# Kernel optimization log

Hardware: AMD Instinct MI355X
Metric: run time of the kernel (lower is better)

Reference implementation:

```python
import jax, jax.numpy as jnp
import numpy as np

B, T, C, H = 4, 2048, 768, 12
D = C // H  # head dim = 64


def setup_inputs() -> dict:
    key = jax.random.key(0)
    ks = jax.random.split(key, 4)
    scale = 0.02
    return {
        "x": jax.random.normal(ks[0], (B, T, C), dtype=jnp.float32),
        "W_attn": jax.random.normal(ks[1], (C, 3 * C), dtype=jnp.float32) * scale,
        "b_attn": jnp.zeros((3 * C,), dtype=jnp.float32),
        "W_proj": jax.random.normal(ks[2], (C, C), dtype=jnp.float32) * scale,
        "b_proj": jnp.zeros((C,), dtype=jnp.float32),
    }


def reference(x, W_attn, b_attn, W_proj, b_proj):
    Bsz, Tlen, Cdim = x.shape
    qkv = x @ W_attn + b_attn                    # [B,T,3C]
    q, k, v = jnp.split(qkv, 3, axis=-1)          # each [B,T,C]
    # [B,T,C] -> [B,H,T,D]
    def heads(t):
        return t.reshape(Bsz, Tlen, H, D).transpose(0, 2, 1, 3)
    q, k, v = heads(q), heads(k), heads(v)
    att = jnp.einsum("bhqd,bhkd->bhqk", q, k) * (1.0 / np.sqrt(D))
    # causal mask: position q attends to k <= q
    mask = jnp.tril(jnp.ones((Tlen, Tlen), dtype=bool))
    att = jnp.where(mask[None, None], att, -jnp.inf)
    att = jax.nn.softmax(att, axis=-1)
    y = jnp.einsum("bhqk,bhkd->bhqd", att, v)     # [B,H,T,D]
    y = y.transpose(0, 2, 1, 3).reshape(Bsz, Tlen, Cdim)
    return y @ W_proj + b_proj
```

## Files before the change

kernel.cpp:

```cpp
#include <hip/hip_runtime.h>

#define B_SZ   4
#define T_LEN  2048
#define C_DIM  768
#define H_NUM  12
#define THREEC (3 * C_DIM)

typedef _Float16 f16;
typedef _Float16 half8 __attribute__((ext_vector_type(8)));
typedef _Float16 half4 __attribute__((ext_vector_type(4)));
typedef __fp16   pk2   __attribute__((ext_vector_type(2)));
typedef float    f32x4 __attribute__((ext_vector_type(4)));

#define GLD16(gaddr, laddr)                                                         \
  __builtin_amdgcn_global_load_lds(                                                 \
      (const __attribute__((address_space(1))) unsigned int*)(gaddr),               \
      (__attribute__((address_space(3))) unsigned int*)(laddr), 16, 0, 0)
#define MFMA16(a, b, c) __builtin_amdgcn_mfma_f32_16x16x32_f16(a, b, c, 0, 0, 0)

__global__ __launch_bounds__(256) void cast_f32_f16_kernel(
    const float* __restrict__ src, f16* __restrict__ dst, int n8) {
  int i = blockIdx.x * 256 + threadIdx.x;
  if (i >= n8) return;
  const float* s = src + (size_t)i * 8;
  half8 h;
#pragma unroll
  for (int u = 0; u < 8; ++u) h[u] = (f16)s[u];
  *(half8*)(dst + (size_t)i * 8) = h;
}

__global__ __launch_bounds__(256) void transpose_cast2_kernel(
    const float* __restrict__ Wa, const float* __restrict__ Wp,
    f16* __restrict__ WtA, f16* __restrict__ WtP) {
  __shared__ f16 tile[32][33];
  int bx = blockIdx.x;
  const float* W; f16* Wt; int N;
  if (bx < THREEC / 32) { W = Wa; Wt = WtA; N = THREEC; }
  else { W = Wp; Wt = WtP; N = C_DIM; bx -= THREEC / 32; }
  const int n0 = bx * 32, k0 = blockIdx.y * 32;
  const int tx = threadIdx.x & 31, ty = threadIdx.x >> 5;
#pragma unroll
  for (int i = 0; i < 4; ++i)
    tile[ty + i * 8][tx] = (f16)W[(size_t)(k0 + ty + i * 8) * N + n0 + tx];
  __syncthreads();
#pragma unroll
  for (int i = 0; i < 4; ++i)
    Wt[(size_t)(n0 + ty + i * 8) * C_DIM + k0 + tx] = tile[tx][ty + i * 8];
}

template <int BM, int BN, int OUT_F16>
__global__ __launch_bounds__(256) void gemm_f16_kernel(
    const f16* __restrict__ A, const f16* __restrict__ Bt,
    const float* __restrict__ bias, f16* __restrict__ OutH,
    float* __restrict__ OutF, int M, int N, int K) {
  __shared__ f16 As[BM * 64];
  __shared__ f16 Bs[BN * 64];
  const int tid = threadIdx.x;
  const int lane = tid & 63, wave = tid >> 6;
  const int lm = lane & 15, kq = lane >> 4, lm7 = lm & 7;
  constexpr int MT = BM / 32, NT = BN / 32;
  const int wm = (wave & 1) * (BM / 2), wn = (wave >> 1) * (BN / 2);
  const int row0 = blockIdx.y * BM, col0 = blockIdx.x * BN;

  f32x4 acc[MT][NT] = {};

  for (int k0 = 0; k0 < K; k0 += 64) {
    __syncthreads();
#pragma unroll
    for (int i = 0; i < BM / 32; ++i) {
      int c = tid + i * 256;
      int r = c >> 3, cc = (c & 7) ^ (r & 7);
      GLD16(&A[(size_t)(row0 + r) * K + k0 + cc * 8],
            &As[(i * 256 + wave * 64) * 8]);
    }
#pragma unroll
    for (int i = 0; i < BN / 32; ++i) {
      int c = tid + i * 256;
      int r = c >> 3, cc = (c & 7) ^ (r & 7);
      GLD16(&Bt[(size_t)(col0 + r) * K + k0 + cc * 8],
            &Bs[(i * 256 + wave * 64) * 8]);
    }
    __syncthreads();
#pragma unroll
    for (int ks = 0; ks < 2; ++ks) {
      const int pos = (ks * 4 + kq);
      half8 af[MT], bf[NT];
#pragma unroll
      for (int t = 0; t < MT; ++t)
        af[t] = *(const half8*)&As[(wm + t * 16 + lm) * 64 + (pos ^ lm7) * 8];
#pragma unroll
      for (int t = 0; t < NT; ++t)
        bf[t] = *(const half8*)&Bs[(wn + t * 16 + lm) * 64 + (pos ^ lm7) * 8];
#pragma unroll
      for (int mt = 0; mt < MT; ++mt)
#pragma unroll
        for (int nt = 0; nt < NT; ++nt)
          acc[mt][nt] = MFMA16(af[mt], bf[nt], acc[mt][nt]);
    }
  }

#pragma unroll
  for (int mt = 0; mt < MT; ++mt) {
    const int row = row0 + wm + mt * 16 + kq * 4;
#pragma unroll
    for (int nt = 0; nt < NT; ++nt) {
      const int col = col0 + wn + nt * 16 + lm;
      const float bv = bias[col];
#pragma unroll
      for (int r = 0; r < 4; ++r) {
        float v = acc[mt][nt][r] + bv;
        if (OUT_F16)
          OutH[(size_t)(row + r) * N + col] = (f16)v;
        else
          OutF[(size_t)(row + r) * N + col] = v;
      }
    }
  }
}

__global__ __launch_bounds__(256) void v_transpose_kernel(
    const f16* __restrict__ qkv, f16* __restrict__ vt) {
  __shared__ f16 tile[64 * 68];
  const int bh = blockIdx.x, b = bh / H_NUM, h = bh % H_NUM;
  const int t0 = blockIdx.y * 64;
  const int tid = threadIdx.x;
#pragma unroll
  for (int i = 0; i < 2; ++i) {
    int c = tid + i * 256;
    int tr = c >> 3, doff = (c & 7) * 8;
    half8 v = *(const half8*)&qkv[(size_t)(b * T_LEN + t0 + tr) * THREEC + 2 * C_DIM + h * 64 + doff];
#pragma unroll
    for (int u = 0; u < 8; ++u) tile[(doff + u) * 68 + tr] = v[u];
  }
  __syncthreads();
#pragma unroll
  for (int i = 0; i < 2; ++i) {
    int c = tid + i * 256;
    int d = c >> 3, toff = (c & 7) * 8;
    half8 v;
#pragma unroll
    for (int u = 0; u < 8; ++u) v[u] = tile[d * 68 + toff + u];
    *(half8*)&vt[((size_t)bh * 64 + d) * T_LEN + t0 + toff] = v;
  }
}

__global__ __launch_bounds__(512, 6) void attn_kernel(
    const f16* __restrict__ qkv, const f16* __restrict__ vt,
    f16* __restrict__ y) {
  __shared__ f16 Kt[2][64 * 64];
  __shared__ f16 Vt[2][64 * 64];
  __shared__ f16 Pl[8][16 * 64];

  const int bh = blockIdx.x, b = bh / H_NUM, h = bh % H_NUM;
  const int yb = blockIdx.y;
  const int qb = 15 - yb;
  const int tid = threadIdx.x, lane = tid & 63, wave = tid >> 6;
  const int lm = lane & 15, kq = lane >> 4, lm7 = lm & 7;
  const int cw = qb * 2 + (wave >> 2);
  const int qw = cw * 64 + (wave & 3) * 16;
  const f16 qscale = (f16)(0.125f * 1.44269504f);

  half8 vones;
#pragma unroll
  for (int u = 0; u < 8; ++u) vones[u] = (f16)1.f;

  half8 bq[2];
#pragma unroll
  for (int c2 = 0; c2 < 2; ++c2) {
    half8 v = *(const half8*)&qkv[(size_t)(b * T_LEN + qw + lm) * THREEC +
                                  h * 64 + c2 * 32 + kq * 8];
    bq[c2] = v * qscale;
  }

  f32x4 o[4] = {};
  f32x4 ol = {};

  f32x4 fz = {};
  asm volatile("" : "+v"(fz));

  const int srow = tid >> 3;
  const int scol = ((tid & 7) ^ (srow & 7)) * 8;
  const f16* kp = &qkv[(size_t)(b * T_LEN + srow) * THREEC + C_DIM + h * 64 + scol];
  const f16* vp = &vt[((size_t)bh * 64 + srow) * T_LEN + scol];

  f16* prow = &Pl[wave][lm * 64];
  const int sbase = wave * 512;

  const int n_tiles = qb * 2 + 2;

  GLD16(kp, &Kt[0][sbase]);
  kp += (size_t)64 * THREEC;
  GLD16(vp, &Vt[0][sbase]);
  vp += 64;

  for (int it = 0; it < n_tiles; ++it) {
    const int cur = it & 1;
    if (it + 1 < n_tiles) {
      GLD16(kp, &Kt[cur ^ 1][sbase]);
      kp += (size_t)64 * THREEC;
      GLD16(vp, &Vt[cur ^ 1][sbase]);
      vp += 64;
      asm volatile("s_waitcnt vmcnt(2)" ::: "memory");
    } else {
      asm volatile("s_waitcnt vmcnt(0)" ::: "memory");
    }
    __builtin_amdgcn_s_barrier();

    if (it <= cw) {
      f32x4 s4[4];
#pragma unroll
      for (int ct = 0; ct < 4; ++ct) {
        const f16* kr = &Kt[cur][(ct * 16 + lm) * 64];
        half8 ak0 = *(const half8*)&kr[(kq ^ lm7) * 8];
        half8 ak1 = *(const half8*)&kr[((4 + kq) ^ lm7) * 8];
        f32x4 z = MFMA16(ak0, bq[0], fz);
        s4[ct] = MFMA16(ak1, bq[1], z);
      }
      if (it == cw) {
        const int qrow = qw + lm, j0 = it * 64;
#pragma unroll
        for (int ct = 0; ct < 4; ++ct)
#pragma unroll
          for (int r = 0; r < 4; ++r)
            if (j0 + ct * 16 + kq * 4 + r > qrow) s4[ct][r] = -1e30f;
      }
#pragma unroll
      for (int ct = 0; ct < 4; ++ct) {
        union { half4 h4; pk2 p2[2]; } u;
        u.p2[0] = __builtin_amdgcn_cvt_pkrtz(
            __builtin_amdgcn_exp2f(s4[ct][0]), __builtin_amdgcn_exp2f(s4[ct][1]));
        u.p2[1] = __builtin_amdgcn_cvt_pkrtz(
            __builtin_amdgcn_exp2f(s4[ct][2]), __builtin_amdgcn_exp2f(s4[ct][3]));
        *(half4*)&prow[(((ct * 2 + (kq >> 1)) ^ lm7) * 8) + (kq & 1) * 4] = u.h4;
      }
      __asm__ volatile("s_waitcnt lgkmcnt(0)" ::: "memory");
      half8 ap0 = *(const half8*)&prow[(kq ^ lm7) * 8];
      half8 ap1 = *(const half8*)&prow[((4 + kq) ^ lm7) * 8];
#pragma unroll
      for (int dt = 0; dt < 4; ++dt) {
        const f16* vr = &Vt[cur][(dt * 16 + lm) * 64];
        half8 bv0 = *(const half8*)&vr[(kq ^ lm7) * 8];
        half8 bv1 = *(const half8*)&vr[((4 + kq) ^ lm7) * 8];
        o[dt] = MFMA16(ap0, bv0, o[dt]);
        o[dt] = MFMA16(ap1, bv1, o[dt]);
      }
      ol = MFMA16(ap0, vones, ol);
      ol = MFMA16(ap1, vones, ol);
    }

    __builtin_amdgcn_s_barrier();
  }

#pragma unroll
  for (int r = 0; r < 4; ++r) {
    const float inv = 1.f / ol[r];
    const size_t base =
        (size_t)(b * T_LEN + qw + kq * 4 + r) * C_DIM + h * 64;
#pragma unroll
    for (int dt = 0; dt < 4; ++dt)
      y[base + dt * 16 + lm] = (f16)(o[dt][r] * inv);
  }
}

extern "C" void kernel_launch(void* const* d_in, const int* in_sizes, int n_in,
                              void* d_out, int out_size, void* d_ws, size_t ws_size,
                              hipStream_t stream) {
  const float* x      = (const float*)d_in[0];
  const float* W_attn = (const float*)d_in[1];
  const float* b_attn = (const float*)d_in[2];
  const float* W_proj = (const float*)d_in[3];
  const float* b_proj = (const float*)d_in[4];
  float* out = (float*)d_out;

  const int M = B_SZ * T_LEN;
  auto align256 = [](size_t v) { return (v + 255) & ~(size_t)255; };
  char* ws = (char*)d_ws;
  f16* xh   = (f16*)ws; ws += align256((size_t)M * C_DIM * 2);
  f16* WtA  = (f16*)ws; ws += align256((size_t)THREEC * C_DIM * 2);
  f16* WtP  = (f16*)ws; ws += align256((size_t)C_DIM * C_DIM * 2);
  f16* qkvh = (f16*)ws; ws += align256((size_t)M * THREEC * 2);
  f16* vtg  = (f16*)ws; ws += align256((size_t)B_SZ * H_NUM * 64 * T_LEN * 2);
  f16* yh   = (f16*)ws; ws += align256((size_t)M * C_DIM * 2);

  {
    int n8 = M * C_DIM / 8;
    cast_f32_f16_kernel<<<(n8 + 255) / 256, 256, 0, stream>>>(x, xh, n8);
  }
  transpose_cast2_kernel<<<dim3((THREEC + C_DIM) / 32, C_DIM / 32), 256, 0, stream>>>(
      W_attn, W_proj, WtA, WtP);

  gemm_f16_kernel<128, 128, 1><<<dim3(THREEC / 128, M / 128), 256, 0, stream>>>(
      xh, WtA, b_attn, qkvh, nullptr, M, THREEC, C_DIM);

  v_transpose_kernel<<<dim3(B_SZ * H_NUM, T_LEN / 64), 256, 0, stream>>>(qkvh, vtg);

  attn_kernel<<<dim3(B_SZ * H_NUM, 16), 512, 0, stream>>>(qkvh, vtg, yh);

  gemm_f16_kernel<128, 64, 0><<<dim3(C_DIM / 64, M / 128), 256, 0, stream>>>(
      yh, WtP, b_proj, nullptr, out, M, C_DIM, C_DIM);
}
```

Baseline: 198.0 us.

## Keep softmax probabilities in registers by permuting V key order

Removes the per-wave LDS round trip for the probability tile. Exponentiated scores now go straight into the MFMA A operand registers, and the key-dimension order mismatch is absorbed by permuting the column positions in the V transpose kernel. This removes the LDS stores, the lgkmcnt wait and the loads in the inner loop, and frees 16KB of shared memory. The occupancy hint is raised from 6 to 8, which adds register pressure.

```diff
diff --git a/kernel.cpp b/kernel.cpp
--- a/kernel.cpp
+++ b/kernel.cpp
@@ -128,9 +128,11 @@
   for (int i = 0; i < 2; ++i) {
     int c = tid + i * 256;
     int tr = c >> 3, doff = (c & 7) * 8;
+    int pcol = ((tr >> 5) << 5) | (((tr >> 2) & 3) << 3) |
+               (((tr >> 4) & 1) << 2) | (tr & 3);
     half8 v = *(const half8*)&qkv[(size_t)(b * T_LEN + t0 + tr) * THREEC + 2 * C_DIM + h * 64 + doff];
 #pragma unroll
-    for (int u = 0; u < 8; ++u) tile[(doff + u) * 68 + tr] = v[u];
+    for (int u = 0; u < 8; ++u) tile[(doff + u) * 68 + pcol] = v[u];
   }
   __syncthreads();
 #pragma unroll
@@ -144,12 +146,11 @@
   }
 }
 
-__global__ __launch_bounds__(512, 6) void attn_kernel(
+__global__ __launch_bounds__(512, 8) void attn_kernel(
     const f16* __restrict__ qkv, const f16* __restrict__ vt,
     f16* __restrict__ y) {
   __shared__ f16 Kt[2][64 * 64];
   __shared__ f16 Vt[2][64 * 64];
-  __shared__ f16 Pl[8][16 * 64];
 
   const int bh = blockIdx.x, b = bh / H_NUM, h = bh % H_NUM;
   const int yb = blockIdx.y;
@@ -183,7 +184,6 @@
   const f16* kp = &qkv[(size_t)(b * T_LEN + srow) * THREEC + C_DIM + h * 64 + scol];
   const f16* vp = &vt[((size_t)bh * 64 + srow) * T_LEN + scol];
 
-  f16* prow = &Pl[wave][lm * 64];
   const int sbase = wave * 512;
 
   const int n_tiles = qb * 2 + 2;
@@ -224,28 +224,34 @@
           for (int r = 0; r < 4; ++r)
             if (j0 + ct * 16 + kq * 4 + r > qrow) s4[ct][r] = -1e30f;
       }
-#pragma unroll
-      for (int ct = 0; ct < 4; ++ct) {
-        union { half4 h4; pk2 p2[2]; } u;
-        u.p2[0] = __builtin_amdgcn_cvt_pkrtz(
-            __builtin_amdgcn_exp2f(s4[ct][0]), __builtin_amdgcn_exp2f(s4[ct][1]));
-        u.p2[1] = __builtin_amdgcn_cvt_pkrtz(
-            __builtin_amdgcn_exp2f(s4[ct][2]), __builtin_amdgcn_exp2f(s4[ct][3]));
-        *(half4*)&prow[(((ct * 2 + (kq >> 1)) ^ lm7) * 8) + (kq & 1) * 4] = u.h4;
-      }
-      __asm__ volatile("s_waitcnt lgkmcnt(0)" ::: "memory");
-      half8 ap0 = *(const half8*)&prow[(kq ^ lm7) * 8];
-      half8 ap1 = *(const half8*)&prow[((4 + kq) ^ lm7) * 8];
+      union { half8 h8; pk2 p2[4]; } pa0, pa1;
+      pa0.p2[0] = __builtin_amdgcn_cvt_pkrtz(
+          __builtin_amdgcn_exp2f(s4[0][0]), __builtin_amdgcn_exp2f(s4[0][1]));
+      pa0.p2[1] = __builtin_amdgcn_cvt_pkrtz(
+          __builtin_amdgcn_exp2f(s4[0][2]), __builtin_amdgcn_exp2f(s4[0][3]));
+      pa0.p2[2] = __builtin_amdgcn_cvt_pkrtz(
+          __builtin_amdgcn_exp2f(s4[1][0]), __builtin_amdgcn_exp2f(s4[1][1]));
+      pa0.p2[3] = __builtin_amdgcn_cvt_pkrtz(
+          __builtin_amdgcn_exp2f(s4[1][2]), __builtin_amdgcn_exp2f(s4[1][3]));
+      pa1.p2[0] = __builtin_amdgcn_cvt_pkrtz(
+          __builtin_amdgcn_exp2f(s4[2][0]), __builtin_amdgcn_exp2f(s4[2][1]));
+      pa1.p2[1] = __builtin_amdgcn_cvt_pkrtz(
+          __builtin_amdgcn_exp2f(s4[2][2]), __builtin_amdgcn_exp2f(s4[2][3]));
+      pa1.p2[2] = __builtin_amdgcn_cvt_pkrtz(
+          __builtin_amdgcn_exp2f(s4[3][0]), __builtin_amdgcn_exp2f(s4[3][1]));
+      pa1.p2[3] = __builtin_amdgcn_cvt_pkrtz(
+          __builtin_amdgcn_exp2f(s4[3][2]), __builtin_amdgcn_exp2f(s4[3][3]));
+
 #pragma unroll
       for (int dt = 0; dt < 4; ++dt) {
         const f16* vr = &Vt[cur][(dt * 16 + lm) * 64];
         half8 bv0 = *(const half8*)&vr[(kq ^ lm7) * 8];
         half8 bv1 = *(const half8*)&vr[((4 + kq) ^ lm7) * 8];
-        o[dt] = MFMA16(ap0, bv0, o[dt]);
-        o[dt] = MFMA16(ap1, bv1, o[dt]);
+        o[dt] = MFMA16(pa0.h8, bv0, o[dt]);
+        o[dt] = MFMA16(pa1.h8, bv1, o[dt]);
       }
-      ol = MFMA16(ap0, vones, ol);
-      ol = MFMA16(ap1, vones, ol);
+      ol = MFMA16(pa0.h8, vones, ol);
+      ol = MFMA16(pa1.h8, vones, ol);
     }
 
     __builtin_amdgcn_s_barrier();
```

Result: no change. 194.4 us (-1.8%).
